# Kernel tuning notes

Measured on AMD Instinct MI355X. Metric: run time of the kernel, lower is better.

The kernel has to match this reference:

```python
import jax, jax.numpy as jnp
import numpy as np

E, H, I, T, K = 8, 2048, 768, 1024, 2


def setup_inputs() -> dict:
    key = jax.random.key(0)
    k1, k2, k3, k4, k5 = jax.random.split(key, 5)
    hidden_states = jax.random.normal(k1, (T, H), jnp.float32)
    routing_weights = jax.random.uniform(k2, (T, K), jnp.float32)
    selected_experts = jax.random.randint(k3, (T, K), 0, E, jnp.int32)
    gate_up_proj = jax.random.normal(k4, (E, H, 2 * I), jnp.float32) * 0.02
    down_proj = jax.random.normal(k5, (E, I, H), jnp.float32) * 0.02
    return {
        "hidden_states": hidden_states,
        "routing_weights": routing_weights,
        "gate_up_proj": gate_up_proj,
        "down_proj": down_proj,
        "selected_experts": selected_experts,
    }


def _grouped_gemm(x, w, expert_ids):
    # x: [N, k], w: [E, k, d], expert_ids: [N] (sorted by expert).
    # Dense-masked grouped GEMM: accumulate each expert's masked matmul.
    n = x.shape[0]
    acc0 = jnp.zeros((n, w.shape[-1]), x.dtype)

    def step(acc, ew):
        e, we = ew
        xm = jnp.where((expert_ids == e)[:, None], x, jnp.zeros((), x.dtype))
        return acc + xm @ we, None

    acc, _ = jax.lax.scan(step, acc0, (jnp.arange(w.shape[0]), w))
    return acc


def reference(hidden_states, routing_weights, gate_up_proj, down_proj, selected_experts):
    t, h = hidden_states.shape
    k = selected_experts.shape[1]
    flat = selected_experts.reshape(-1)                     # [T*K]
    sort_idx = jnp.argsort(flat)                            # stable sort by expert id (permute)
    token_idx = sort_idx // k                               # source token per permuted row
    permuted = hidden_states[token_idx]                     # [T*K, H]
    experts_sorted = flat[sort_idx]                         # [T*K]

    fc1 = _grouped_gemm(permuted, gate_up_proj, experts_sorted)   # [T*K, 2I]
    a, b = jnp.split(fc1, 2, axis=-1)
    act = jax.nn.silu(a) * b                                # npu_swiglu
    fc2 = _grouped_gemm(act, down_proj, experts_sorted)     # [T*K, H]

    inv = jnp.argsort(sort_idx)                             # unpermute map (row_ids_map)
    unperm = fc2[inv].reshape(t, k, h)                      # [T, K, H]
    return jnp.einsum('tkh,tk->th', unperm, routing_weights)
```

## Files before the change

kernel.cpp:

```cpp
#include <hip/hip_runtime.h>
#include <math.h>

#define E_  8
#define H_  2048
#define I_  768
#define T_  1024
#define K_  2
#define TK_ 2048
#define GU_ 1536

typedef short  short8 __attribute__((ext_vector_type(8)));
typedef __bf16 bf16x8 __attribute__((ext_vector_type(8)));
typedef float  f32x4  __attribute__((ext_vector_type(4)));

static __device__ __forceinline__ short f2bf(float f) {
  union { float f; unsigned u; } v; v.f = f;
  unsigned r = (v.u + 0x7fffu + ((v.u >> 16) & 1u)) >> 16;
  return (short)r;
}

#define GLOAD_LDS16(g, l)                                                   \
  __builtin_amdgcn_global_load_lds(                                         \
      (const __attribute__((address_space(1))) void*)(g),                   \
      (__attribute__((address_space(3))) void*)(l), 16, 0, 0)

__global__ __launch_bounds__(256) void route_kernel(
    const int* __restrict__ sel, int* __restrict__ offs,
    int* __restrict__ rows, int* __restrict__ inv) {
  __shared__ int cnt[E_], cur[E_], loff[E_ + 1];
  int t = threadIdx.x;
  if (t < E_) { cnt[t] = 0; cur[t] = 0; }
  __syncthreads();
  for (int p = t; p < TK_; p += 256) atomicAdd(&cnt[sel[p]], 1);
  __syncthreads();
  if (t == 0) {
    int s = 0;
    for (int e = 0; e < E_; ++e) { loff[e] = s; s += cnt[e]; }
    loff[E_] = s;
  }
  __syncthreads();
  if (t <= E_) offs[t] = loff[t];
  for (int p = t; p < TK_; p += 256) {
    int e = sel[p];
    int pos = loff[e] + atomicAdd(&cur[e], 1);
    rows[pos] = p;
    inv[p] = pos;
  }
}

__global__ __launch_bounds__(256) void xcast_kernel(
    const float* __restrict__ X, unsigned short* __restrict__ Xb) {
  int i = blockIdx.x * 256 + threadIdx.x;
  float4 v = ((const float4*)X)[i];
  ushort4 o;
  o.x = (unsigned short)f2bf(v.x); o.y = (unsigned short)f2bf(v.y);
  o.z = (unsigned short)f2bf(v.z); o.w = (unsigned short)f2bf(v.w);
  ((ushort4*)Xb)[i] = o;
}

__global__ __launch_bounds__(256) void wtrans_kernel(
    const float* __restrict__ src, unsigned short* __restrict__ dst,
    int K, int N) {
  __shared__ __align__(16) unsigned short tile[64][72];
  int b  = blockIdx.z;
  int k0 = blockIdx.x * 64, n0 = blockIdx.y * 64;
  const float* s = src + (size_t)b * K * N;
  unsigned short* d = dst + (size_t)b * N * K;
  int t = threadIdx.x;
  int kr = t >> 4;
  int nc = (t & 15) * 4;
#pragma unroll
  for (int it = 0; it < 4; ++it) {
    int kk = kr + it * 16;
    float4 v = *(const float4*)(s + (size_t)(k0 + kk) * N + n0 + nc);
    tile[nc + 0][kk] = (unsigned short)f2bf(v.x);
    tile[nc + 1][kk] = (unsigned short)f2bf(v.y);
    tile[nc + 2][kk] = (unsigned short)f2bf(v.z);
    tile[nc + 3][kk] = (unsigned short)f2bf(v.w);
  }
  __syncthreads();
#pragma unroll
  for (int it = 0; it < 2; ++it) {
    int c = it * 256 + t;
    int onr = c >> 3, ok = (c & 7) * 8;
    short8 vv = *(const short8*)&tile[onr][ok];
    *(short8*)(d + (size_t)(n0 + onr) * K + k0 + ok) = vv;
  }
}

__global__ __launch_bounds__(256) void fc1_mfma(
    const unsigned short* __restrict__ Xb, const unsigned short* __restrict__ GUPt,
    const int* __restrict__ offs, const int* __restrict__ rows,
    unsigned short* __restrict__ act) {
  __shared__ __align__(16) unsigned short As[64 * 32];
  __shared__ __align__(16) unsigned short Bs[128 * 32];

  int e    = blockIdx.y >> 5;
  int rbeg = offs[e], rend = offs[e + 1];
  int row0 = rbeg + (blockIdx.y & 31) * 64;
  if (row0 >= rend) return;
  int col0 = blockIdx.x * 64;

  int tid = threadIdx.x, lane = tid & 63, w = tid >> 6;

  int ar   = w * 16 + (lane >> 2);
  int aidx = row0 + ar; if (aidx > rend - 1) aidx = rend - 1;
  int tok  = rows[aidx] >> 1;
  const unsigned short* agp = Xb + (size_t)tok * H_ + (lane & 3) * 8;
  unsigned short* aldst = As + w * 16 * 32;

  const unsigned short* gupe = GUPt + (size_t)e * GU_ * H_;
  int br0 = w * 32 + (lane >> 2), br1 = br0 + 16;
  int n0g = (br0 < 64) ? (col0 + br0) : (I_ + col0 + br0 - 64);
  int n1g = (br1 < 64) ? (col0 + br1) : (I_ + col0 + br1 - 64);
  const unsigned short* bgp0 = gupe + (size_t)n0g * H_ + (lane & 3) * 8;
  const unsigned short* bgp1 = gupe + (size_t)n1g * H_ + (lane & 3) * 8;
  unsigned short* bldst0 = Bs + (w * 32) * 32;
  unsigned short* bldst1 = Bs + (w * 32 + 16) * 32;

  f32x4 acc[4][2] = {};
  int m = lane & 15, q = lane >> 4;

  for (int k0 = 0; k0 < H_; k0 += 32) {
    GLOAD_LDS16(agp  + k0, aldst);
    GLOAD_LDS16(bgp0 + k0, bldst0);
    GLOAD_LDS16(bgp1 + k0, bldst1);
    __syncthreads();
    bf16x8 af[4], bfr[2];
#pragma unroll
    for (int mt = 0; mt < 4; ++mt)
      af[mt] = *(const bf16x8*)(As + (mt * 16 + m) * 32 + q * 8);
    bfr[0] = *(const bf16x8*)(Bs + (w * 16 + m) * 32 + q * 8);
    bfr[1] = *(const bf16x8*)(Bs + (64 + w * 16 + m) * 32 + q * 8);
#pragma unroll
    for (int mt = 0; mt < 4; ++mt) {
      acc[mt][0] = __builtin_amdgcn_mfma_f32_16x16x32_bf16(af[mt], bfr[0], acc[mt][0], 0, 0, 0);
      acc[mt][1] = __builtin_amdgcn_mfma_f32_16x16x32_bf16(af[mt], bfr[1], acc[mt][1], 0, 0, 0);
    }
    __syncthreads();
  }

#pragma unroll
  for (int mt = 0; mt < 4; ++mt)
#pragma unroll
    for (int r = 0; r < 4; ++r) {
      int prow = row0 + mt * 16 + q * 4 + r;
      if (prow < rend) {
        float g = acc[mt][0][r], u = acc[mt][1][r];
        float a = g / (1.0f + __expf(-g)) * u;
        act[(size_t)prow * I_ + col0 + w * 16 + m] = (unsigned short)f2bf(a);
      }
    }
}

__global__ __launch_bounds__(256) void fc2_mfma(
    const unsigned short* __restrict__ act, const unsigned short* __restrict__ DWNt,
    const int* __restrict__ offs, float* __restrict__ fc2buf) {
  __shared__ __align__(16) unsigned short As[64 * 32];
  __shared__ __align__(16) unsigned short Bs[128 * 32];

  int e    = blockIdx.y >> 5;
  int rbeg = offs[e], rend = offs[e + 1];
  int row0 = rbeg + (blockIdx.y & 31) * 64;
  if (row0 >= rend) return;
  int col0 = blockIdx.x * 128;

  int tid = threadIdx.x, lane = tid & 63, w = tid >> 6;

  int ar   = w * 16 + (lane >> 2);
  int aidx = row0 + ar; if (aidx > TK_ - 1) aidx = TK_ - 1;
  const unsigned short* agp = act + (size_t)aidx * I_ + (lane & 3) * 8;
  unsigned short* aldst = As + w * 16 * 32;

  const unsigned short* dwe = DWNt + (size_t)e * H_ * I_;
  int br0 = w * 32 + (lane >> 2), br1 = br0 + 16;
  const unsigned short* bgp0 = dwe + (size_t)(col0 + br0) * I_ + (lane & 3) * 8;
  const unsigned short* bgp1 = dwe + (size_t)(col0 + br1) * I_ + (lane & 3) * 8;
  unsigned short* bldst0 = Bs + (w * 32) * 32;
  unsigned short* bldst1 = Bs + (w * 32 + 16) * 32;

  f32x4 acc[4][2] = {};
  int m = lane & 15, q = lane >> 4;

  for (int k0 = 0; k0 < I_; k0 += 32) {
    GLOAD_LDS16(agp  + k0, aldst);
    GLOAD_LDS16(bgp0 + k0, bldst0);
    GLOAD_LDS16(bgp1 + k0, bldst1);
    __syncthreads();
    bf16x8 af[4], bfr[2];
#pragma unroll
    for (int mt = 0; mt < 4; ++mt)
      af[mt] = *(const bf16x8*)(As + (mt * 16 + m) * 32 + q * 8);
    bfr[0] = *(const bf16x8*)(Bs + (w * 16 + m) * 32 + q * 8);
    bfr[1] = *(const bf16x8*)(Bs + (64 + w * 16 + m) * 32 + q * 8);
#pragma unroll
    for (int mt = 0; mt < 4; ++mt) {
      acc[mt][0] = __builtin_amdgcn_mfma_f32_16x16x32_bf16(af[mt], bfr[0], acc[mt][0], 0, 0, 0);
      acc[mt][1] = __builtin_amdgcn_mfma_f32_16x16x32_bf16(af[mt], bfr[1], acc[mt][1], 0, 0, 0);
    }
    __syncthreads();
  }

#pragma unroll
  for (int mt = 0; mt < 4; ++mt)
#pragma unroll
    for (int nf = 0; nf < 2; ++nf)
#pragma unroll
      for (int r = 0; r < 4; ++r) {
        int prow = row0 + mt * 16 + q * 4 + r;
        if (prow < rend)
          fc2buf[(size_t)prow * H_ + col0 + nf * 64 + w * 16 + m] = acc[mt][nf][r];
      }
}

__global__ __launch_bounds__(256) void combine_kernel(
    const float* __restrict__ fc2buf, const float* __restrict__ RW,
    const int* __restrict__ inv, float* __restrict__ out) {
  int idx = blockIdx.x * 256 + threadIdx.x;
  int t = idx >> 9, c4 = idx & 511;
  if (t >= T_) return;
  int r0 = inv[t * 2], r1 = inv[t * 2 + 1];
  float w0 = RW[t * 2], w1 = RW[t * 2 + 1];
  float4 v0 = ((const float4*)(fc2buf + (size_t)r0 * H_))[c4];
  float4 v1 = ((const float4*)(fc2buf + (size_t)r1 * H_))[c4];
  float4 o;
  o.x = w0 * v0.x + w1 * v1.x;
  o.y = w0 * v0.y + w1 * v1.y;
  o.z = w0 * v0.z + w1 * v1.z;
  o.w = w0 * v0.w + w1 * v1.w;
  ((float4*)(out + (size_t)t * H_))[c4] = o;
}

__global__ __launch_bounds__(256) void fc1_kernel(
    const float* __restrict__ X, const float* __restrict__ GUP,
    const int* __restrict__ offs, const int* __restrict__ rows,
    unsigned short* __restrict__ act) {
  __shared__ __align__(16) short As[64][40];
  __shared__ __align__(16) short Bs[64][40];
  int e    = blockIdx.y >> 5;
  int rbeg = offs[e], rend = offs[e + 1];
  int row0 = rbeg + (blockIdx.y & 31) * 64;
  if (row0 >= rend) return;
  int col0 = blockIdx.x * 32;
  int tid = threadIdx.x, lane = tid & 63, w = tid >> 6;
  int ar = tid >> 2, akc = (tid & 3) * 8;
  int aprow = row0 + ar;
  bool avalid = aprow < rend;
  const float* xrow = avalid ? (X + (size_t)(rows[aprow] >> 1) * H_) : X;
  int bn = tid & 63, bo = (tid >> 6) * 8;
  int gcol = (bn < 32) ? (col0 + bn) : (I_ + col0 + (bn - 32));
  const float* bbase = GUP + (size_t)e * H_ * GU_ + gcol;
  f32x4 acc[4] = {};
  for (int k0 = 0; k0 < H_; k0 += 32) {
    float4 v0, v1;
    if (avalid) {
      const float4* p = (const float4*)(xrow + k0 + akc);
      v0 = p[0]; v1 = p[1];
    } else { v0 = make_float4(0.f,0.f,0.f,0.f); v1 = v0; }
    short8 sv;
    sv[0]=f2bf(v0.x); sv[1]=f2bf(v0.y); sv[2]=f2bf(v0.z); sv[3]=f2bf(v0.w);
    sv[4]=f2bf(v1.x); sv[5]=f2bf(v1.y); sv[6]=f2bf(v1.z); sv[7]=f2bf(v1.w);
    *(short8*)&As[ar][akc] = sv;
    const float* bp = bbase + (size_t)(k0 + bo) * GU_;
    short8 bv;
#pragma unroll
    for (int j = 0; j < 8; ++j) bv[j] = f2bf(bp[(size_t)j * GU_]);
    *(short8*)&Bs[bn][bo] = bv;
    __syncthreads();
    bf16x8 af = *(const bf16x8*)&As[w * 16 + (lane & 15)][(lane >> 4) * 8];
#pragma unroll
    for (int nt = 0; nt < 4; ++nt) {
      bf16x8 bf = *(const bf16x8*)&Bs[nt * 16 + (lane & 15)][(lane >> 4) * 8];
      acc[nt] = __builtin_amdgcn_mfma_f32_16x16x32_bf16(af, bf, acc[nt], 0, 0, 0);
    }
    __syncthreads();
  }
  int n = lane & 15, q = lane >> 4;
#pragma unroll
  for (int nt = 0; nt < 2; ++nt)
#pragma unroll
    for (int r = 0; r < 4; ++r) {
      int prow = row0 + w * 16 + q * 4 + r;
      if (prow < rend) {
        float g = acc[nt][r], u = acc[nt + 2][r];
        float a = g / (1.0f + __expf(-g)) * u;
        act[(size_t)prow * I_ + col0 + nt * 16 + n] = (unsigned short)f2bf(a);
      }
    }
}

__global__ __launch_bounds__(256) void fc2_kernel(
    const unsigned short* __restrict__ act, const float* __restrict__ DWN,
    const float* __restrict__ RW,
    const int* __restrict__ offs, const int* __restrict__ rows,
    float* __restrict__ fc2buf, float* __restrict__ outAtomic, int mode) {
  __shared__ __align__(16) short As[64][40];
  __shared__ __align__(16) short Bs[64][40];
  int e    = blockIdx.y >> 5;
  int rbeg = offs[e], rend = offs[e + 1];
  int row0 = rbeg + (blockIdx.y & 31) * 64;
  if (row0 >= rend) return;
  int col0 = blockIdx.x * 64;
  int tid = threadIdx.x, lane = tid & 63, w = tid >> 6;
  int ar = tid >> 2, akc = (tid & 3) * 8;
  int aprow = row0 + ar;
  bool avalid = aprow < rend;
  const unsigned short* arow = act + (size_t)(avalid ? aprow : row0) * I_;
  int bn = tid & 63, bo = (tid >> 6) * 8;
  const float* bbase = DWN + (size_t)e * I_ * H_ + col0 + bn;
  f32x4 acc[4] = {};
  for (int k0 = 0; k0 < I_; k0 += 32) {
    short8 av;
    if (avalid) av = *(const short8*)(arow + k0 + akc);
    else        av = (short8){0,0,0,0,0,0,0,0};
    *(short8*)&As[ar][akc] = av;
    const float* bp = bbase + (size_t)(k0 + bo) * H_;
    short8 bv;
#pragma unroll
    for (int j = 0; j < 8; ++j) bv[j] = f2bf(bp[(size_t)j * H_]);
    *(short8*)&Bs[bn][bo] = bv;
    __syncthreads();
    bf16x8 af = *(const bf16x8*)&As[w * 16 + (lane & 15)][(lane >> 4) * 8];
#pragma unroll
    for (int nt = 0; nt < 4; ++nt) {
      bf16x8 bf = *(const bf16x8*)&Bs[nt * 16 + (lane & 15)][(lane >> 4) * 8];
      acc[nt] = __builtin_amdgcn_mfma_f32_16x16x32_bf16(af, bf, acc[nt], 0, 0, 0);
    }
    __syncthreads();
  }
  int n = lane & 15, q = lane >> 4;
  if (mode == 0) {
#pragma unroll
    for (int nt = 0; nt < 4; ++nt)
#pragma unroll
      for (int r = 0; r < 4; ++r) {
        int prow = row0 + w * 16 + q * 4 + r;
        if (prow < rend)
          fc2buf[(size_t)prow * H_ + col0 + nt * 16 + n] = acc[nt][r];
      }
  } else {
#pragma unroll
    for (int nt = 0; nt < 4; ++nt)
#pragma unroll
      for (int r = 0; r < 4; ++r) {
        int prow = row0 + w * 16 + q * 4 + r;
        if (prow < rend) {
          int pair = rows[prow];
          float rw = RW[pair];
          atomicAdd(&outAtomic[(size_t)(pair >> 1) * H_ + col0 + nt * 16 + n],
                    rw * acc[nt][r]);
        }
      }
  }
}

__global__ __launch_bounds__(256) void zero_kernel(float* __restrict__ out, int n) {
  int i = blockIdx.x * 256 + threadIdx.x;
  if (i < n) out[i] = 0.f;
}

extern "C" void kernel_launch(void* const* d_in, const int* in_sizes, int n_in,
                              void* d_out, int out_size, void* d_ws, size_t ws_size,
                              hipStream_t stream) {
  const float* X   = (const float*)d_in[0];
  const float* RW  = (const float*)d_in[1];
  const float* GUP = (const float*)d_in[2];
  const float* DWN = (const float*)d_in[3];
  const int*   SEL = (const int*)d_in[4];
  float* out = (float*)d_out;

  char* ws = (char*)d_ws;
  int* offs = (int*)ws;
  int* rows = (int*)(ws + 1024);
  int* inv  = (int*)(ws + 16384);
  unsigned short* Xb   = (unsigned short*)(ws + 32768);
  unsigned short* GUPt = (unsigned short*)(ws + 32768 + 4194304);
  unsigned short* DWNt = (unsigned short*)(ws + 32768 + 4194304 + 50331648);
  unsigned short* act  = (unsigned short*)(ws + 32768 + 4194304 + 50331648 + 25165824);
  float* fc2buf = (float*)(ws + 32768 + 4194304 + 50331648 + 25165824 + 3145728);
  size_t fast_need = 32768ull + 4194304 + 50331648 + 25165824 + 3145728 + 16777216;

  hipLaunchKernelGGL(route_kernel, dim3(1), dim3(256), 0, stream, SEL, offs, rows, inv);

  if (ws_size >= fast_need) {
    hipLaunchKernelGGL(xcast_kernel, dim3(T_ * H_ / 4 / 256), dim3(256), 0, stream, X, Xb);
    hipLaunchKernelGGL(wtrans_kernel, dim3(H_ / 64, GU_ / 64, E_), dim3(256), 0, stream,
                       GUP, GUPt, H_, GU_);
    hipLaunchKernelGGL(wtrans_kernel, dim3(I_ / 64, H_ / 64, E_), dim3(256), 0, stream,
                       DWN, DWNt, I_, H_);
    hipLaunchKernelGGL(fc1_mfma, dim3(12, 256), dim3(256), 0, stream,
                       Xb, GUPt, offs, rows, act);
    hipLaunchKernelGGL(fc2_mfma, dim3(16, 256), dim3(256), 0, stream,
                       act, DWNt, offs, fc2buf);
    hipLaunchKernelGGL(combine_kernel, dim3(T_ * 2), dim3(256), 0, stream,
                       fc2buf, RW, inv, out);
  } else {
    unsigned short* act2 = (unsigned short*)(ws + 32768);
    float* fc2buf2 = (float*)(ws + 32768 + (size_t)TK_ * I_ * 2);
    size_t need = 32768 + (size_t)TK_ * I_ * 2 + (size_t)TK_ * H_ * 4;
    int mode = (ws_size >= need) ? 0 : 1;
    hipLaunchKernelGGL(fc1_kernel, dim3(24, 256), dim3(256), 0, stream,
                       X, GUP, offs, rows, act2);
    if (mode == 1)
      hipLaunchKernelGGL(zero_kernel, dim3((T_ * H_ + 255) / 256), dim3(256), 0, stream,
                         out, T_ * H_);
    hipLaunchKernelGGL(fc2_kernel, dim3(32, 256), dim3(256), 0, stream,
                       act2, DWN, RW, offs, rows, fc2buf2, out, mode);
    if (mode == 0)
      hipLaunchKernelGGL(combine_kernel, dim3(T_ * 2), dim3(256), 0, stream,
                         fc2buf2, RW, inv, out);
  }
}
```

Baseline: 301.7 us.

## Double-buffer MFMA GEMMs with XOR-swizzled LDS and smaller tiles

Both grouped GEMM kernels now load 64-wide K slices into double-buffered LDS with an XOR swizzle, so the global-to-LDS copy of the next slice overlaps compute and one barrier per iteration is dropped. Output tiles shrink (fc1 64x32 paired gate/up columns, fc2 64x64) and the grids double, which raises occupancy at the cost of lower data reuse per block. The weight transpose/cast kernel and the activation cast use packed bf16 conversion with a swizzled LDS tile. The new conversion rounds half up rather than to nearest even, which can change the last bit of some bf16 values.

```diff
diff --git a/kernel.cpp b/kernel.cpp
--- a/kernel.cpp
+++ b/kernel.cpp
@@ -19,10 +19,23 @@
   return (short)r;
 }
 
+static __device__ __forceinline__ unsigned pk2bf(float a, float b) {
+  unsigned ua = __float_as_uint(a) + 0x8000u;
+  unsigned ub = __float_as_uint(b) + 0x8000u;
+  return __builtin_amdgcn_perm(ub, ua, 0x07060302u);
+}
+
 #define GLOAD_LDS16(g, l)                                                   \
   __builtin_amdgcn_global_load_lds(                                         \
       (const __attribute__((address_space(1))) void*)(g),                   \
       (__attribute__((address_space(3))) void*)(l), 16, 0, 0)
+
+#define MFMA_BF16_16x16x32 __builtin_amdgcn_mfma_f32_16x16x32_bf16
+
+static __device__ __forceinline__ bf16x8 frag_ld(const unsigned short* base,
+                                                 int row, int oct) {
+  return *(const bf16x8*)(base + row * 64 + ((oct ^ (row & 7)) * 8));
+}
 
 __global__ __launch_bounds__(256) void route_kernel(
     const int* __restrict__ sel, int* __restrict__ offs,
@@ -52,39 +65,42 @@
     const float* __restrict__ X, unsigned short* __restrict__ Xb) {
   int i = blockIdx.x * 256 + threadIdx.x;
   float4 v = ((const float4*)X)[i];
-  ushort4 o;
-  o.x = (unsigned short)f2bf(v.x); o.y = (unsigned short)f2bf(v.y);
-  o.z = (unsigned short)f2bf(v.z); o.w = (unsigned short)f2bf(v.w);
-  ((ushort4*)Xb)[i] = o;
+  unsigned p0 = pk2bf(v.x, v.y), p1 = pk2bf(v.z, v.w);
+  ((uint2*)Xb)[i] = make_uint2(p0, p1);
 }
 
 __global__ __launch_bounds__(256) void wtrans_kernel(
     const float* __restrict__ src, unsigned short* __restrict__ dst,
     int K, int N) {
-  __shared__ __align__(16) unsigned short tile[64][72];
+  __shared__ __align__(16) unsigned short tile[64 * 64];
   int b  = blockIdx.z;
   int k0 = blockIdx.x * 64, n0 = blockIdx.y * 64;
-  const float* s = src + (size_t)b * K * N;
-  unsigned short* d = dst + (size_t)b * N * K;
+  const float* s = src + (size_t)b * K * N + (size_t)k0 * N + n0;
+  unsigned short* d = dst + (size_t)b * N * K + (size_t)n0 * K + k0;
   int t = threadIdx.x;
-  int kr = t >> 4;
-  int nc = (t & 15) * 4;
-#pragma unroll
-  for (int it = 0; it < 4; ++it) {
-    int kk = kr + it * 16;
-    float4 v = *(const float4*)(s + (size_t)(k0 + kk) * N + n0 + nc);
-    tile[nc + 0][kk] = (unsigned short)f2bf(v.x);
-    tile[nc + 1][kk] = (unsigned short)f2bf(v.y);
-    tile[nc + 2][kk] = (unsigned short)f2bf(v.z);
-    tile[nc + 3][kk] = (unsigned short)f2bf(v.w);
+  int kq = (t >> 4) * 4;
+  int nq = (t & 15) * 4;
+  float4 v[4];
+#pragma unroll
+  for (int i = 0; i < 4; ++i)
+    v[i] = *(const float4*)(s + (size_t)(kq + i) * N + nq);
+  int qlog = kq >> 2;
+#pragma unroll
+  for (int j = 0; j < 4; ++j) {
+    int n = nq + j;
+    unsigned p0 = pk2bf(((const float*)&v[0])[j], ((const float*)&v[1])[j]);
+    unsigned p1 = pk2bf(((const float*)&v[2])[j], ((const float*)&v[3])[j]);
+    int qphys = qlog ^ (n & 15);
+    *(uint2*)(tile + n * 64 + qphys * 4) = make_uint2(p0, p1);
   }
   __syncthreads();
-#pragma unroll
-  for (int it = 0; it < 2; ++it) {
-    int c = it * 256 + t;
-    int onr = c >> 3, ok = (c & 7) * 8;
-    short8 vv = *(const short8*)&tile[onr][ok];
-    *(short8*)(d + (size_t)(n0 + onr) * K + k0 + ok) = vv;
+  int r = t >> 2;
+#pragma unroll
+  for (int p = 0; p < 2; ++p) {
+    int q0 = (t & 3) * 4 + p * 2;
+    uint2 a_ = *(const uint2*)(tile + r * 64 + ((q0 ^ (r & 15)) * 4));
+    uint2 b2 = *(const uint2*)(tile + r * 64 + (((q0 + 1) ^ (r & 15)) * 4));
+    *(uint4*)(d + (size_t)r * K + q0 * 4) = make_uint4(a_.x, a_.y, b2.x, b2.y);
   }
 }
 
@@ -92,63 +108,75 @@
     const unsigned short* __restrict__ Xb, const unsigned short* __restrict__ GUPt,
     const int* __restrict__ offs, const int* __restrict__ rows,
     unsigned short* __restrict__ act) {
-  __shared__ __align__(16) unsigned short As[64 * 32];
-  __shared__ __align__(16) unsigned short Bs[128 * 32];
+  __shared__ __align__(16) unsigned short As[2][64 * 64];
+  __shared__ __align__(16) unsigned short Bs[2][64 * 64];
 
   int e    = blockIdx.y >> 5;
   int rbeg = offs[e], rend = offs[e + 1];
   int row0 = rbeg + (blockIdx.y & 31) * 64;
   if (row0 >= rend) return;
-  int col0 = blockIdx.x * 64;
+  int c0 = blockIdx.x * 32;
 
   int tid = threadIdx.x, lane = tid & 63, w = tid >> 6;
-
-  int ar   = w * 16 + (lane >> 2);
-  int aidx = row0 + ar; if (aidx > rend - 1) aidx = rend - 1;
-  int tok  = rows[aidx] >> 1;
-  const unsigned short* agp = Xb + (size_t)tok * H_ + (lane & 3) * 8;
-  unsigned short* aldst = As + w * 16 * 32;
+  int rl  = lane >> 3;
+  int oct = (lane & 7) ^ rl;
+
+  int arow0 = row0 + w * 16 + rl, arow1 = arow0 + 8;
+  int aidx0 = arow0 < rend ? arow0 : rend - 1;
+  int aidx1 = arow1 < rend ? arow1 : rend - 1;
+  const unsigned short* agp0 = Xb + (size_t)(rows[aidx0] >> 1) * H_ + oct * 8;
+  const unsigned short* agp1 = Xb + (size_t)(rows[aidx1] >> 1) * H_ + oct * 8;
 
   const unsigned short* gupe = GUPt + (size_t)e * GU_ * H_;
-  int br0 = w * 32 + (lane >> 2), br1 = br0 + 16;
-  int n0g = (br0 < 64) ? (col0 + br0) : (I_ + col0 + br0 - 64);
-  int n1g = (br1 < 64) ? (col0 + br1) : (I_ + col0 + br1 - 64);
-  const unsigned short* bgp0 = gupe + (size_t)n0g * H_ + (lane & 3) * 8;
-  const unsigned short* bgp1 = gupe + (size_t)n1g * H_ + (lane & 3) * 8;
-  unsigned short* bldst0 = Bs + (w * 32) * 32;
-  unsigned short* bldst1 = Bs + (w * 32 + 16) * 32;
-
-  f32x4 acc[4][2] = {};
+  int br0 = w * 16 + rl, br1 = br0 + 8;
+  int n0 = (br0 < 32) ? (c0 + br0) : (I_ + c0 + br0 - 32);
+  int n1 = (br1 < 32) ? (c0 + br1) : (I_ + c0 + br1 - 32);
+  const unsigned short* bgp0 = gupe + (size_t)n0 * H_ + oct * 8;
+  const unsigned short* bgp1 = gupe + (size_t)n1 * H_ + oct * 8;
+
+  auto issue = [&](int buf, int k0) {
+    GLOAD_LDS16(agp0 + k0, &As[buf][0] + (w * 16) * 64);
+    GLOAD_LDS16(agp1 + k0, &As[buf][0] + (w * 16 + 8) * 64);
+    GLOAD_LDS16(bgp0 + k0, &Bs[buf][0] + (w * 16) * 64);
+    GLOAD_LDS16(bgp1 + k0, &Bs[buf][0] + (w * 16 + 8) * 64);
+  };
+
+  int mh = w >> 1, nh = w & 1;
   int m = lane & 15, q = lane >> 4;
-
-  for (int k0 = 0; k0 < H_; k0 += 32) {
-    GLOAD_LDS16(agp  + k0, aldst);
-    GLOAD_LDS16(bgp0 + k0, bldst0);
-    GLOAD_LDS16(bgp1 + k0, bldst1);
-    __syncthreads();
-    bf16x8 af[4], bfr[2];
-#pragma unroll
-    for (int mt = 0; mt < 4; ++mt)
-      af[mt] = *(const bf16x8*)(As + (mt * 16 + m) * 32 + q * 8);
-    bfr[0] = *(const bf16x8*)(Bs + (w * 16 + m) * 32 + q * 8);
-    bfr[1] = *(const bf16x8*)(Bs + (64 + w * 16 + m) * 32 + q * 8);
-#pragma unroll
-    for (int mt = 0; mt < 4; ++mt) {
-      acc[mt][0] = __builtin_amdgcn_mfma_f32_16x16x32_bf16(af[mt], bfr[0], acc[mt][0], 0, 0, 0);
-      acc[mt][1] = __builtin_amdgcn_mfma_f32_16x16x32_bf16(af[mt], bfr[1], acc[mt][1], 0, 0, 0);
-    }
-    __syncthreads();
-  }
-
-#pragma unroll
-  for (int mt = 0; mt < 4; ++mt)
+  f32x4 acc[2][2] = {};
+
+  issue(0, 0);
+  int cur = 0;
+  const int niter = H_ / 64;
+#pragma unroll 1
+  for (int it = 0; it < niter; ++it) {
+    __syncthreads();
+    if (it + 1 < niter) issue(cur ^ 1, (it + 1) * 64);
+    const unsigned short* a_ = &As[cur][0];
+    const unsigned short* b_ = &Bs[cur][0];
+#pragma unroll
+    for (int kk = 0; kk < 2; ++kk) {
+      bf16x8 af0 = frag_ld(a_, mh * 32 + m,      kk * 4 + q);
+      bf16x8 af1 = frag_ld(a_, mh * 32 + 16 + m, kk * 4 + q);
+      bf16x8 bg  = frag_ld(b_, nh * 16 + m,      kk * 4 + q);
+      bf16x8 bu  = frag_ld(b_, 32 + nh * 16 + m, kk * 4 + q);
+      acc[0][0] = MFMA_BF16_16x16x32(af0, bg, acc[0][0], 0, 0, 0);
+      acc[0][1] = MFMA_BF16_16x16x32(af0, bu, acc[0][1], 0, 0, 0);
+      acc[1][0] = MFMA_BF16_16x16x32(af1, bg, acc[1][0], 0, 0, 0);
+      acc[1][1] = MFMA_BF16_16x16x32(af1, bu, acc[1][1], 0, 0, 0);
+    }
+    cur ^= 1;
+  }
+
+#pragma unroll
+  for (int mt = 0; mt < 2; ++mt)
 #pragma unroll
     for (int r = 0; r < 4; ++r) {
-      int prow = row0 + mt * 16 + q * 4 + r;
+      int prow = row0 + mh * 32 + mt * 16 + q * 4 + r;
       if (prow < rend) {
         float g = acc[mt][0][r], u = acc[mt][1][r];
         float a = g / (1.0f + __expf(-g)) * u;
-        act[(size_t)prow * I_ + col0 + w * 16 + m] = (unsigned short)f2bf(a);
+        act[(size_t)prow * I_ + c0 + nh * 16 + m] = (unsigned short)f2bf(a);
       }
     }
 }
@@ -156,60 +184,72 @@
 __global__ __launch_bounds__(256) void fc2_mfma(
     const unsigned short* __restrict__ act, const unsigned short* __restrict__ DWNt,
     const int* __restrict__ offs, float* __restrict__ fc2buf) {
-  __shared__ __align__(16) unsigned short As[64 * 32];
-  __shared__ __align__(16) unsigned short Bs[128 * 32];
+  __shared__ __align__(16) unsigned short As[2][64 * 64];
+  __shared__ __align__(16) unsigned short Bs[2][64 * 64];
 
   int e    = blockIdx.y >> 5;
   int rbeg = offs[e], rend = offs[e + 1];
   int row0 = rbeg + (blockIdx.y & 31) * 64;
   if (row0 >= rend) return;
-  int col0 = blockIdx.x * 128;
+  int c0 = blockIdx.x * 64;
 
   int tid = threadIdx.x, lane = tid & 63, w = tid >> 6;
-
-  int ar   = w * 16 + (lane >> 2);
-  int aidx = row0 + ar; if (aidx > TK_ - 1) aidx = TK_ - 1;
-  const unsigned short* agp = act + (size_t)aidx * I_ + (lane & 3) * 8;
-  unsigned short* aldst = As + w * 16 * 32;
+  int rl  = lane >> 3;
+  int oct = (lane & 7) ^ rl;
+
+  int arow0 = row0 + w * 16 + rl, arow1 = arow0 + 8;
+  int aidx0 = arow0 < rend ? arow0 : rend - 1;
+  int aidx1 = arow1 < rend ? arow1 : rend - 1;
+  const unsigned short* agp0 = act + (size_t)aidx0 * I_ + oct * 8;
+  const unsigned short* agp1 = act + (size_t)aidx1 * I_ + oct * 8;
 
   const unsigned short* dwe = DWNt + (size_t)e * H_ * I_;
-  int br0 = w * 32 + (lane >> 2), br1 = br0 + 16;
-  const unsigned short* bgp0 = dwe + (size_t)(col0 + br0) * I_ + (lane & 3) * 8;
-  const unsigned short* bgp1 = dwe + (size_t)(col0 + br1) * I_ + (lane & 3) * 8;
-  unsigned short* bldst0 = Bs + (w * 32) * 32;
-  unsigned short* bldst1 = Bs + (w * 32 + 16) * 32;
-
-  f32x4 acc[4][2] = {};
+  const unsigned short* bgp0 = dwe + (size_t)(c0 + w * 16 + rl) * I_ + oct * 8;
+  const unsigned short* bgp1 = dwe + (size_t)(c0 + w * 16 + rl + 8) * I_ + oct * 8;
+
+  auto issue = [&](int buf, int k0) {
+    GLOAD_LDS16(agp0 + k0, &As[buf][0] + (w * 16) * 64);
+    GLOAD_LDS16(agp1 + k0, &As[buf][0] + (w * 16 + 8) * 64);
+    GLOAD_LDS16(bgp0 + k0, &Bs[buf][0] + (w * 16) * 64);
+    GLOAD_LDS16(bgp1 + k0, &Bs[buf][0] + (w * 16 + 8) * 64);
+  };
+
+  int mh = w >> 1, nh = w & 1;
   int m = lane & 15, q = lane >> 4;
-
-  for (int k0 = 0; k0 < I_; k0 += 32) {
-    GLOAD_LDS16(agp  + k0, aldst);
-    GLOAD_LDS16(bgp0 + k0, bldst0);
-    GLOAD_LDS16(bgp1 + k0, bldst1);
-    __syncthreads();
-    bf16x8 af[4], bfr[2];
-#pragma unroll
-    for (int mt = 0; mt < 4; ++mt)
-      af[mt] = *(const bf16x8*)(As + (mt * 16 + m) * 32 + q * 8);
-    bfr[0] = *(const bf16x8*)(Bs + (w * 16 + m) * 32 + q * 8);
-    bfr[1] = *(const bf16x8*)(Bs + (64 + w * 16 + m) * 32 + q * 8);
-#pragma unroll
-    for (int mt = 0; mt < 4; ++mt) {
-      acc[mt][0] = __builtin_amdgcn_mfma_f32_16x16x32_bf16(af[mt], bfr[0], acc[mt][0], 0, 0, 0);
-      acc[mt][1] = __builtin_amdgcn_mfma_f32_16x16x32_bf16(af[mt], bfr[1], acc[mt][1], 0, 0, 0);
-    }
-    __syncthreads();
-  }
-
-#pragma unroll
-  for (int mt = 0; mt < 4; ++mt)
-#pragma unroll
-    for (int nf = 0; nf < 2; ++nf)
+  f32x4 acc[2][2] = {};
+
+  issue(0, 0);
+  int cur = 0;
+  const int niter = I_ / 64;
+#pragma unroll 1
+  for (int it = 0; it < niter; ++it) {
+    __syncthreads();
+    if (it + 1 < niter) issue(cur ^ 1, (it + 1) * 64);
+    const unsigned short* a_ = &As[cur][0];
+    const unsigned short* b_ = &Bs[cur][0];
+#pragma unroll
+    for (int kk = 0; kk < 2; ++kk) {
+      bf16x8 af0 = frag_ld(a_, mh * 32 + m,          kk * 4 + q);
+      bf16x8 af1 = frag_ld(a_, mh * 32 + 16 + m,     kk * 4 + q);
+      bf16x8 bf0 = frag_ld(b_, nh * 32 + m,          kk * 4 + q);
+      bf16x8 bf1 = frag_ld(b_, nh * 32 + 16 + m,     kk * 4 + q);
+      acc[0][0] = MFMA_BF16_16x16x32(af0, bf0, acc[0][0], 0, 0, 0);
+      acc[0][1] = MFMA_BF16_16x16x32(af0, bf1, acc[0][1], 0, 0, 0);
+      acc[1][0] = MFMA_BF16_16x16x32(af1, bf0, acc[1][0], 0, 0, 0);
+      acc[1][1] = MFMA_BF16_16x16x32(af1, bf1, acc[1][1], 0, 0, 0);
+    }
+    cur ^= 1;
+  }
+
+#pragma unroll
+  for (int mt = 0; mt < 2; ++mt)
+#pragma unroll
+    for (int nt = 0; nt < 2; ++nt)
 #pragma unroll
       for (int r = 0; r < 4; ++r) {
-        int prow = row0 + mt * 16 + q * 4 + r;
+        int prow = row0 + mh * 32 + mt * 16 + q * 4 + r;
         if (prow < rend)
-          fc2buf[(size_t)prow * H_ + col0 + nf * 64 + w * 16 + m] = acc[mt][nf][r];
+          fc2buf[(size_t)prow * H_ + c0 + nh * 32 + nt * 16 + m] = acc[mt][nt][r];
       }
 }
 
@@ -271,7 +311,7 @@
 #pragma unroll
     for (int nt = 0; nt < 4; ++nt) {
       bf16x8 bf = *(const bf16x8*)&Bs[nt * 16 + (lane & 15)][(lane >> 4) * 8];
-      acc[nt] = __builtin_amdgcn_mfma_f32_16x16x32_bf16(af, bf, acc[nt], 0, 0, 0);
+      acc[nt] = MFMA_BF16_16x16x32(af, bf, acc[nt], 0, 0, 0);
     }
     __syncthreads();
   }
@@ -324,7 +364,7 @@
 #pragma unroll
     for (int nt = 0; nt < 4; ++nt) {
       bf16x8 bf = *(const bf16x8*)&Bs[nt * 16 + (lane & 15)][(lane >> 4) * 8];
-      acc[nt] = __builtin_amdgcn_mfma_f32_16x16x32_bf16(af, bf, acc[nt], 0, 0, 0);
+      acc[nt] = MFMA_BF16_16x16x32(af, bf, acc[nt], 0, 0, 0);
     }
     __syncthreads();
   }
@@ -388,9 +428,9 @@
                        GUP, GUPt, H_, GU_);
     hipLaunchKernelGGL(wtrans_kernel, dim3(I_ / 64, H_ / 64, E_), dim3(256), 0, stream,
                        DWN, DWNt, I_, H_);
-    hipLaunchKernelGGL(fc1_mfma, dim3(12, 256), dim3(256), 0, stream,
+    hipLaunchKernelGGL(fc1_mfma, dim3(24, 256), dim3(256), 0, stream,
                        Xb, GUPt, offs, rows, act);
-    hipLaunchKernelGGL(fc2_mfma, dim3(16, 256), dim3(256), 0, stream,
+    hipLaunchKernelGGL(fc2_mfma, dim3(32, 256), dim3(256), 0, stream,
                        act, DWNt, offs, fc2buf);
     hipLaunchKernelGGL(combine_kernel, dim3(T_ * 2), dim3(256), 0, stream,
                        fc2buf, RW, inv, out);
```

Result: faster. 264.7 us (-12.3%).
